# Kernel optimization log

Hardware: AMD Instinct MI355X
Metric: run time of the kernel (lower is better)

The kernel has to match this reference:

```python
import jax, jax.numpy as jnp
import numpy as np
from functools import partial

# Block hyperparams (match init_kwargs)
B, C, N, H = 16, 512, 1024, 8
HID = 4 * C
TAU, THRESH, SG_SCALE = 2.0, 1.0, 5.0
ATTN_SCALE = 0.25
BN_EPS = 1e-5

# LIF spiking neuron (single-step, stateless): membrane v = x / tau, hard threshold
# forward; sigmoid surrogate gradient (scale=5.0) in backward.
@partial(jax.custom_vjp, nondiff_argnums=(1,))
def spike(u, scale):
    return (u >= 0.0).astype(u.dtype)

def _spike_fwd(u, scale):
    return spike(u, scale), u

def _spike_bwd(scale, u, g):
    s = jax.nn.sigmoid(scale * u)
    return (g * scale * s * (1.0 - s),)

spike.defvjp(_spike_fwd, _spike_bwd)

def lif(x):
    return spike(x / TAU - THRESH, SG_SCALE)

def conv1x1(x, w, b=None):
    # x: [B,C,N], w: [O,C] -> [B,O,N]
    y = jnp.einsum('oc,bcn->bon', w, x)
    return y if b is None else y + b[None, :, None]

def bn(x, g, b):
    # BatchNorm1d, training-mode batch stats over (batch, length), biased var
    m = jnp.mean(x, axis=(0, 2), keepdims=True)
    v = jnp.var(x, axis=(0, 2), keepdims=True)
    return (x - m) * jax.lax.rsqrt(v + BN_EPS) * g[None, :, None] + b[None, :, None]


def setup_inputs() -> dict:
    key = jax.random.key(0)
    ks = jax.random.split(key, 8)
    w = lambda k, o, i: jax.random.normal(k, (o, i), dtype=jnp.float32) * 0.02
    inp = {
        'x': jax.random.normal(ks[0], (B, C, N), dtype=jnp.float32),
        'q_w': w(ks[1], C, C), 'q_g': jnp.ones((C,), jnp.float32), 'q_b': jnp.zeros((C,), jnp.float32),
        'k_w': w(ks[2], C, C), 'k_g': jnp.ones((C,), jnp.float32), 'k_b': jnp.zeros((C,), jnp.float32),
        'v_w': w(ks[3], C, C), 'v_g': jnp.ones((C,), jnp.float32), 'v_b': jnp.zeros((C,), jnp.float32),
        'proj_w': w(ks[4], C, C), 'proj_bias': jnp.zeros((C,), jnp.float32),
        'proj_g': jnp.ones((C,), jnp.float32), 'proj_b': jnp.zeros((C,), jnp.float32),
        'fc1_w': w(ks[5], HID, C), 'fc1_bias': jnp.zeros((HID,), jnp.float32),
        'fc1_g': jnp.ones((HID,), jnp.float32), 'fc1_b': jnp.zeros((HID,), jnp.float32),
        'fc2_w': w(ks[6], C, HID), 'fc2_bias': jnp.zeros((C,), jnp.float32),
        'fc2_g': jnp.ones((C,), jnp.float32), 'fc2_b': jnp.zeros((C,), jnp.float32),
    }
    return inp


def reference(x, q_w, q_g, q_b, k_w, k_g, k_b, v_w, v_g, v_b,
              proj_w, proj_bias, proj_g, proj_b,
              fc1_w, fc1_bias, fc1_g, fc1_b, fc2_w, fc2_bias, fc2_g, fc2_b):
    Bb, Cc, Nn = x.shape
    D = Cc // H

    def heads(t):  # [B,C,N] -> [B,H,N,D]
        return t.transpose(0, 2, 1).reshape(Bb, Nn, H, D).transpose(0, 2, 1, 3)

    # spiking attention (no softmax): (Q K^T) V * 0.25
    q = heads(lif(bn(conv1x1(x, q_w), q_g, q_b)))
    k = heads(lif(bn(conv1x1(x, k_w), k_g, k_b)))
    v = heads(lif(bn(conv1x1(x, v_w), v_g, v_b)))
    scores = jnp.einsum('bhnd,bhmd->bhnm', q, k)            # [B,H,N,N]
    attn = jnp.einsum('bhnm,bhmd->bhnd', scores, v) * ATTN_SCALE
    a = attn.transpose(0, 1, 3, 2).reshape(Bb, Cc, Nn)       # [B,C,N]
    a = lif(a)
    a = lif(bn(conv1x1(a, proj_w, proj_bias), proj_g, proj_b))
    x = x + a                                                # residual 1

    # conv1x1-BN-LIF MLP
    h = lif(bn(conv1x1(x, fc1_w, fc1_bias), fc1_g, fc1_b))
    h = lif(bn(conv1x1(h, fc2_w, fc2_bias), fc2_g, fc2_b))
    return x + h                                             # residual 2
```

## Files before the change

kernel.cpp:

```cpp
#include <hip/hip_runtime.h>
#include <stdint.h>

#pragma clang fp contract(off)

#define BATCH 16
#define CCH   512
#define NLEN  1024
#define NH    8
#define DH    64

__device__ float pw128(const float* __restrict__ x) {
    float r0=x[0],r1=x[1],r2=x[2],r3=x[3],r4=x[4],r5=x[5],r6=x[6],r7=x[7];
    for (int i = 8; i < 128; i += 8) {
        r0 += x[i+0]; r1 += x[i+1]; r2 += x[i+2]; r3 += x[i+3];
        r4 += x[i+4]; r5 += x[i+5]; r6 += x[i+6]; r7 += x[i+7];
    }
    return ((r0+r1)+(r2+r3))+((r4+r5)+(r6+r7));
}
__device__ float pw128_sqdev(const float* __restrict__ x, float m) {
    float r0,r1,r2,r3,r4,r5,r6,r7;
    {
        float d;
        d = x[0]-m; r0 = d*d;  d = x[1]-m; r1 = d*d;
        d = x[2]-m; r2 = d*d;  d = x[3]-m; r3 = d*d;
        d = x[4]-m; r4 = d*d;  d = x[5]-m; r5 = d*d;
        d = x[6]-m; r6 = d*d;  d = x[7]-m; r7 = d*d;
    }
    for (int i = 8; i < 128; i += 8) {
        float d;
        d = x[i+0]-m; r0 += d*d;  d = x[i+1]-m; r1 += d*d;
        d = x[i+2]-m; r2 += d*d;  d = x[i+3]-m; r3 += d*d;
        d = x[i+4]-m; r4 += d*d;  d = x[i+5]-m; r5 += d*d;
        d = x[i+6]-m; r6 += d*d;  d = x[i+7]-m; r7 += d*d;
    }
    return ((r0+r1)+(r2+r3))+((r4+r5)+(r6+r7));
}

__global__ __launch_bounds__(64) void bn_stats_np_k(const float* __restrict__ Y, int O,
                                                    float2* __restrict__ st)
{
    const int o = blockIdx.x;
    const int t = threadIdx.x;
    __shared__ float part[16];
    __shared__ float msh;
    if (t < 16) {
        const float* p = Y + ((size_t)t * O + o) * NLEN;
        float b0 = pw128(p), b1 = pw128(p+128), b2 = pw128(p+256), b3 = pw128(p+384);
        float b4 = pw128(p+512), b5 = pw128(p+640), b6 = pw128(p+768), b7 = pw128(p+896);
        part[t] = ((b0+b1)+(b2+b3))+((b4+b5)+(b6+b7));
    }
    __syncthreads();
    if (t == 0) {
        float s = part[0];
        for (int b = 1; b < 16; ++b) s += part[b];
        msh = s / 16384.0f;
    }
    __syncthreads();
    const float m = msh;
    if (t < 16) {
        const float* p = Y + ((size_t)t * O + o) * NLEN;
        float b0 = pw128_sqdev(p,     m), b1 = pw128_sqdev(p+128, m);
        float b2 = pw128_sqdev(p+256, m), b3 = pw128_sqdev(p+384, m);
        float b4 = pw128_sqdev(p+512, m), b5 = pw128_sqdev(p+640, m);
        float b6 = pw128_sqdev(p+768, m), b7 = pw128_sqdev(p+896, m);
        part[t] = ((b0+b1)+(b2+b3))+((b4+b5)+(b6+b7));
    }
    __syncthreads();
    if (t == 0) {
        float s = part[0];
        for (int b = 1; b < 16; ++b) s += part[b];
        float var = s / 16384.0f;
        float ve  = var + 1e-5f;
        float sq  = (float)sqrt((double)ve);
        float r   = (float)(1.0 / (double)sq);
        st[o] = make_float2(m, r);
    }
}

__device__ inline bool spike_f32(float y, float2 s, float g, float b) {
    float t1 = y - s.x;
    float t2 = t1 * s.y;
    float t3 = t2 * g;
    float t4 = t3 + b;
    float u  = t4 / 2.0f - 1.0f;
    return u >= 0.0f;
}

template<int MODE>
__global__ __launch_bounds__(512, 2) void gemm_k(
    const float* __restrict__ W, const float* __restrict__ Xf, const uint8_t* __restrict__ Xs8,
    const float* __restrict__ bias, float* __restrict__ Y,
    int O, int Cin, int N)
{
    __shared__ float Ws[32][132];
    __shared__ float Xs[32][132];
    const int b = blockIdx.z;
    const size_t xbase = (size_t)b * Cin * N;
    float* Yb = Y + (size_t)b * O * N;
    const int o0 = blockIdx.y * 128;
    const int n0 = blockIdx.x * 128;
    const int t  = threadIdx.x;
    const int tx = t & 15;
    const int ty = t >> 4;

    const int wr = t >> 2;
    const int wk = (t & 3) << 3;
    const int xk = t >> 4;
    const int xc = (t & 15) << 3;

    float acc[4][8];
#pragma unroll
    for (int i = 0; i < 4; ++i)
#pragma unroll
        for (int j = 0; j < 8; ++j) acc[i][j] = 0.0f;

    float4 wA0, wA1;
    float  xr[8];

    auto loadG = [&](int k0) {
        const float* wp = W + (size_t)(o0 + wr) * Cin + k0 + wk;
        wA0 = *reinterpret_cast<const float4*>(wp);
        wA1 = *reinterpret_cast<const float4*>(wp + 4);
        size_t off = xbase + (size_t)(k0 + xk) * N + n0 + xc;
        if (MODE == 0) {
            float4 v0 = *reinterpret_cast<const float4*>(Xf + off);
            float4 v1 = *reinterpret_cast<const float4*>(Xf + off + 4);
            xr[0]=v0.x; xr[1]=v0.y; xr[2]=v0.z; xr[3]=v0.w;
            xr[4]=v1.x; xr[5]=v1.y; xr[6]=v1.z; xr[7]=v1.w;
        } else {
            float4 v0 = *reinterpret_cast<const float4*>(Xf + off);
            float4 v1 = *reinterpret_cast<const float4*>(Xf + off + 4);
            uchar4 u0 = *reinterpret_cast<const uchar4*>(Xs8 + off);
            uchar4 u1 = *reinterpret_cast<const uchar4*>(Xs8 + off + 4);
            xr[0]=v0.x+(float)u0.x; xr[1]=v0.y+(float)u0.y;
            xr[2]=v0.z+(float)u0.z; xr[3]=v0.w+(float)u0.w;
            xr[4]=v1.x+(float)u1.x; xr[5]=v1.y+(float)u1.y;
            xr[6]=v1.z+(float)u1.z; xr[7]=v1.w+(float)u1.w;
        }
    };
    auto stage = [&]() {
        Ws[wk+0][wr]=wA0.x; Ws[wk+1][wr]=wA0.y; Ws[wk+2][wr]=wA0.z; Ws[wk+3][wr]=wA0.w;
        Ws[wk+4][wr]=wA1.x; Ws[wk+5][wr]=wA1.y; Ws[wk+6][wr]=wA1.z; Ws[wk+7][wr]=wA1.w;
        *reinterpret_cast<float4*>(&Xs[xk][xc])     = make_float4(xr[0],xr[1],xr[2],xr[3]);
        *reinterpret_cast<float4*>(&Xs[xk][xc + 4]) = make_float4(xr[4],xr[5],xr[6],xr[7]);
    };

    loadG(0);
    stage();
    __syncthreads();
    for (int k0 = 0;;) {
        const int kn = k0 + 32;
        const bool more = kn < Cin;
        if (more) loadG(kn);
#pragma unroll
        for (int kk = 0; kk < 32; ++kk) {
            float4 a  = *reinterpret_cast<const float4*>(&Ws[kk][ty * 4]);
            float4 b0 = *reinterpret_cast<const float4*>(&Xs[kk][tx * 4]);
            float4 b1 = *reinterpret_cast<const float4*>(&Xs[kk][64 + tx * 4]);
            float av[4] = {a.x, a.y, a.z, a.w};
            float bv[8] = {b0.x, b0.y, b0.z, b0.w, b1.x, b1.y, b1.z, b1.w};
#pragma unroll
            for (int i = 0; i < 4; ++i)
#pragma unroll
                for (int j = 0; j < 8; ++j)
                    acc[i][j] = fmaf(av[i], bv[j], acc[i][j]);
        }
        if (!more) break;
        __syncthreads();
        stage();
        __syncthreads();
        k0 = kn;
    }
#pragma unroll
    for (int i = 0; i < 4; ++i) {
        const int o = o0 + ty * 4 + i;
        const float bb = bias ? bias[o] : 0.0f;
        float* yp = Yb + (size_t)o * N + n0;
        float4 r0, r1;
        r0.x = acc[i][0] + bb; r0.y = acc[i][1] + bb;
        r0.z = acc[i][2] + bb; r0.w = acc[i][3] + bb;
        r1.x = acc[i][4] + bb; r1.y = acc[i][5] + bb;
        r1.z = acc[i][6] + bb; r1.w = acc[i][7] + bb;
        *reinterpret_cast<float4*>(yp + tx * 4)      = r0;
        *reinterpret_cast<float4*>(yp + 64 + tx * 4) = r1;
    }
}

__global__ __launch_bounds__(256) void wt_k(const float* __restrict__ W, float* __restrict__ Wt,
                                            int O, int Cin)
{
    __shared__ float tile[32][33];
    const int k0 = blockIdx.x * 32, o0 = blockIdx.y * 32;
    const int tx = threadIdx.x & 31, ty = threadIdx.x >> 5;
#pragma unroll
    for (int j = 0; j < 4; ++j)
        tile[ty + 8*j][tx] = W[(size_t)(o0 + ty + 8*j) * Cin + k0 + tx];
    __syncthreads();
#pragma unroll
    for (int j = 0; j < 4; ++j)
        Wt[(size_t)(k0 + ty + 8*j) * O + o0 + tx] = tile[tx][ty + 8*j];
}

__global__ __launch_bounds__(256) void col_bits_k(const uint8_t* __restrict__ S,
                                                  unsigned long long* __restrict__ bits, int Cin)
{
    const int n0 = blockIdx.x * 64, kw = blockIdx.y, b = blockIdx.z;
    __shared__ uint8_t tile[64][64];
    const int t = threadIdx.x;
    const int r = t >> 2, cg = (t & 3) * 16;
    const uint8_t* src = S + ((size_t)b * Cin + kw * 64 + r) * NLEN + n0 + cg;
    *reinterpret_cast<uint4*>(&tile[r][cg]) = *reinterpret_cast<const uint4*>(src);
    __syncthreads();
    if (t < 64) {
        unsigned long long m = 0;
#pragma unroll
        for (int rr = 0; rr < 64; ++rr)
            m |= ((unsigned long long)(tile[rr][t] != 0)) << rr;
        bits[((size_t)b * NLEN + n0 + t) * (Cin >> 6) + kw] = m;
    }
}

__global__ __launch_bounds__(256) void sparse_gemm_k(
    const float* __restrict__ Wt, const unsigned long long* __restrict__ bits,
    const float* __restrict__ bias, float* __restrict__ Y, int Cin)
{
    const int wid  = (blockIdx.x << 2) + (threadIdx.x >> 6);
    const int lane = threadIdx.x & 63;
    const int b = wid >> 10, n = wid & 1023;
    const int W64 = Cin >> 6;
    float acc[8];
#pragma unroll
    for (int i = 0; i < 8; ++i) acc[i] = 0.0f;
    const unsigned long long* bp = bits + ((size_t)b * NLEN + n) * W64;
    for (int w = 0; w < W64; ++w) {
        unsigned long long m = bp[w];
        while (m) {
            const int bit = __builtin_ctzll(m);
            m &= m - 1;
            const int k = (w << 6) + bit;
            const float* wr = Wt + ((size_t)k << 9) + lane * 8;
            float4 w0 = *reinterpret_cast<const float4*>(wr);
            float4 w1 = *reinterpret_cast<const float4*>(wr + 4);
            acc[0] += w0.x; acc[1] += w0.y; acc[2] += w0.z; acc[3] += w0.w;
            acc[4] += w1.x; acc[5] += w1.y; acc[6] += w1.z; acc[7] += w1.w;
        }
    }
    const float* bq = bias + lane * 8;
    float4 b0 = *reinterpret_cast<const float4*>(bq);
    float4 b1 = *reinterpret_cast<const float4*>(bq + 4);
    float bi[8] = {b0.x, b0.y, b0.z, b0.w, b1.x, b1.y, b1.z, b1.w};
    float* yp = Y + ((size_t)b * 512 + lane * 8) * NLEN + n;
#pragma unroll
    for (int i = 0; i < 8; ++i)
        yp[(size_t)i * NLEN] = acc[i] + bi[i];
}

__global__ __launch_bounds__(256) void spike_pack_k(
    const float* __restrict__ Y, const float2* __restrict__ st,
    const float* __restrict__ g, const float* __restrict__ bet,
    uint8_t* __restrict__ out)
{
    const int nt = blockIdx.x, h = blockIdx.y, b = blockIdx.z;
    __shared__ uint8_t tile[64][68];
    const int t = threadIdx.x;
    {
        const int i = t & 63, dq = t >> 6;
#pragma unroll
        for (int p = 0; p < 16; ++p) {
            int d = dq * 16 + p;
            int c = h * 64 + d;
            float y = Y[((size_t)b * CCH + c) * NLEN + nt * 64 + i];
            tile[d][i] = spike_f32(y, st[c], g[c], bet[c]) ? 1 : 0;
        }
    }
    __syncthreads();
    {
        const int d = t & 63, iq = t >> 6;
#pragma unroll
        for (int p = 0; p < 16; ++p) {
            int i = iq * 16 + p;
            out[((size_t)(b * NH + h) * NLEN + nt * 64 + i) * DH + d] = tile[d][i];
        }
    }
}

__global__ __launch_bounds__(256) void ktv_k(const uint8_t* __restrict__ Kb, const uint8_t* __restrict__ Vb,
                                             float* __restrict__ M)
{
    const int bh = blockIdx.x;
    const uint8_t* kp = Kb + (size_t)bh * NLEN * DH;
    const uint8_t* vp = Vb + (size_t)bh * NLEN * DH;
    __shared__ float ks[64][68];
    __shared__ float vs[64][68];
    const int t = threadIdx.x;
    const int d2 = t & 63, g4 = t >> 6;
    float acc[16];
#pragma unroll
    for (int j = 0; j < 16; ++j) acc[j] = 0.f;

    for (int nc = 0; nc < NLEN; nc += 64) {
#pragma unroll
        for (int p = 0; p < 16; ++p) {
            int idx = t + p * 256;
            int r = idx >> 6, d = idx & 63;
            ks[r][d] = (float)kp[(size_t)(nc + r) * DH + d];
            vs[r][d] = (float)vp[(size_t)(nc + r) * DH + d];
        }
        __syncthreads();
        for (int n = 0; n < 64; ++n) {
            float vv = vs[n][d2];
#pragma unroll
            for (int j = 0; j < 16; ++j)
                acc[j] += ks[n][g4 * 16 + j] * vv;
        }
        __syncthreads();
    }
#pragma unroll
    for (int j = 0; j < 16; ++j)
        M[(size_t)bh * 4096 + (size_t)(g4 * 16 + j) * 64 + d2] = acc[j];
}

__global__ __launch_bounds__(256) void attn_spike_k(const uint8_t* __restrict__ Qb, const float* __restrict__ M,
                                                    uint8_t* __restrict__ A)
{
    const int nt = blockIdx.x, h = blockIdx.y, b = blockIdx.z;
    const int bh = b * NH + h;
    __shared__ float Ms[64][68];
    __shared__ float qs[64][65];
    const int t = threadIdx.x;
#pragma unroll
    for (int p = 0; p < 16; ++p) {
        int idx = t + p * 256;
        int r = idx >> 6, c = idx & 63;
        Ms[r][c] = M[(size_t)bh * 4096 + idx];
        qs[c][r] = (float)Qb[((size_t)bh * NLEN + nt * 64 + r) * DH + c];
    }
    __syncthreads();
    const int n = t & 63, dg = t >> 6;
    float acc[16];
#pragma unroll
    for (int j = 0; j < 16; ++j) acc[j] = 0.f;
    for (int d1 = 0; d1 < 64; ++d1) {
        float qv = qs[d1][n];
#pragma unroll
        for (int j = 0; j < 16; ++j)
            acc[j] += qv * Ms[d1][dg * 16 + j];
    }
#pragma unroll
    for (int j = 0; j < 16; ++j) {
        int d = dg * 16 + j;
        A[((size_t)b * CCH + h * 64 + d) * NLEN + nt * 64 + n] = (acc[j] >= 8.0f) ? 1 : 0;
    }
}

__global__ __launch_bounds__(256) void spike_store_k(
    const float* __restrict__ Y, const float2* __restrict__ st,
    const float* __restrict__ g, const float* __restrict__ bet,
    uint8_t* __restrict__ H, int Oc, int o_off, int Otot)
{
    size_t i4 = (size_t)blockIdx.x * 256 + threadIdx.x;
    size_t total = (size_t)BATCH * Oc * (NLEN / 4);
    if (i4 >= total) return;
    int n4 = (int)(i4 & 255);
    int o  = (int)((i4 >> 8) % Oc);
    int b  = (int)(i4 / ((size_t)256 * Oc));
    float4 y = reinterpret_cast<const float4*>(Y)[i4];
    float2 s = st[o];
    float gg = g[o], bb = bet[o];
    uchar4 r;
    r.x = spike_f32(y.x, s, gg, bb) ? 1 : 0;
    r.y = spike_f32(y.y, s, gg, bb) ? 1 : 0;
    r.z = spike_f32(y.z, s, gg, bb) ? 1 : 0;
    r.w = spike_f32(y.w, s, gg, bb) ? 1 : 0;
    *reinterpret_cast<uchar4*>(H + ((size_t)(b * Otot + o_off + o)) * NLEN + n4 * 4) = r;
}

__global__ __launch_bounds__(256) void final_k(
    const float* __restrict__ Y, const float2* __restrict__ st,
    const float* __restrict__ g, const float* __restrict__ bet,
    const float* __restrict__ x, const uint8_t* __restrict__ ares,
    float* __restrict__ Out)
{
    size_t i4 = (size_t)blockIdx.x * 256 + threadIdx.x;
    size_t total = (size_t)BATCH * CCH * (NLEN / 4);
    if (i4 >= total) return;
    int o = (int)((i4 >> 8) % CCH);
    float4 y  = reinterpret_cast<const float4*>(Y)[i4];
    float4 xv = reinterpret_cast<const float4*>(x)[i4];
    uchar4 av = reinterpret_cast<const uchar4*>(ares)[i4];
    float2 s = st[o];
    float gg = g[o], bb = bet[o];
    float4 r;
    {
        float x1;
        x1 = xv.x + (float)av.x; r.x = x1 + (spike_f32(y.x, s, gg, bb) ? 1.0f : 0.0f);
        x1 = xv.y + (float)av.y; r.y = x1 + (spike_f32(y.y, s, gg, bb) ? 1.0f : 0.0f);
        x1 = xv.z + (float)av.z; r.z = x1 + (spike_f32(y.z, s, gg, bb) ? 1.0f : 0.0f);
        x1 = xv.w + (float)av.w; r.w = x1 + (spike_f32(y.w, s, gg, bb) ? 1.0f : 0.0f);
    }
    reinterpret_cast<float4*>(Out)[i4] = r;
}

extern "C" void kernel_launch(void* const* d_in, const int* in_sizes, int n_in,
                              void* d_out, int out_size, void* d_ws, size_t ws_size,
                              hipStream_t stream)
{
    const float* x         = (const float*)d_in[0];
    const float* q_w       = (const float*)d_in[1];
    const float* q_g       = (const float*)d_in[2];
    const float* q_b       = (const float*)d_in[3];
    const float* k_w       = (const float*)d_in[4];
    const float* k_g       = (const float*)d_in[5];
    const float* k_b       = (const float*)d_in[6];
    const float* v_w       = (const float*)d_in[7];
    const float* v_g       = (const float*)d_in[8];
    const float* v_b       = (const float*)d_in[9];
    const float* proj_w    = (const float*)d_in[10];
    const float* proj_bias = (const float*)d_in[11];
    const float* proj_g    = (const float*)d_in[12];
    const float* proj_b    = (const float*)d_in[13];
    const float* fc1_w     = (const float*)d_in[14];
    const float* fc1_bias  = (const float*)d_in[15];
    const float* fc1_g     = (const float*)d_in[16];
    const float* fc1_b     = (const float*)d_in[17];
    const float* fc2_w     = (const float*)d_in[18];
    const float* fc2_bias  = (const float*)d_in[19];
    const float* fc2_g     = (const float*)d_in[20];
    const float* fc2_b     = (const float*)d_in[21];
    float* out = (float*)d_out;

    char* ws = (char*)d_ws;
    const size_t MiB = 1ull << 20;
    if (ws_size < 124 * MiB) return;

    float*    Af    = (float*)(ws);
    uint8_t*  ab    = (uint8_t*)(ws + 64 * MiB);
    uint8_t*  ares  = (uint8_t*)(ws + 72 * MiB);
    uint8_t*  qb    = (uint8_t*)(ws + 80 * MiB);
    uint8_t*  kb    = (uint8_t*)(ws + 88 * MiB);
    uint8_t*  vb    = (uint8_t*)(ws + 96 * MiB);
    uint8_t*  hb    = (uint8_t*)(ws + 80 * MiB);
    float*    Mbuf  = (float*)(ws + 112 * MiB);
    float2*   stats = (float2*)(ws + 114 * MiB);
    float*    Wt    = (float*)(ws + 115 * MiB);
    unsigned long long* bits = (unsigned long long*)(ws + 119 * MiB);

    dim3 thr256(256), thr512(512);

    const float* Wts[3] = {q_w, k_w, v_w};
    const float* Gt[3]  = {q_g, k_g, v_g};
    const float* Bt[3]  = {q_b, k_b, v_b};
    uint8_t*     Pt[3]  = {qb, kb, vb};
    for (int tsr = 0; tsr < 3; ++tsr) {
        gemm_k<0><<<dim3(8, 4, 16), thr512, 0, stream>>>(Wts[tsr], x, nullptr, nullptr, Af, 512, 512, 1024);
        bn_stats_np_k<<<dim3(512), dim3(64), 0, stream>>>(Af, 512, stats);
        spike_pack_k<<<dim3(16, 8, 16), thr256, 0, stream>>>(Af, stats, Gt[tsr], Bt[tsr], Pt[tsr]);
    }

    ktv_k<<<dim3(128), thr256, 0, stream>>>(kb, vb, Mbuf);
    attn_spike_k<<<dim3(16, 8, 16), thr256, 0, stream>>>(qb, Mbuf, ab);

    wt_k<<<dim3(16, 16), thr256, 0, stream>>>(proj_w, Wt, 512, 512);
    col_bits_k<<<dim3(16, 8, 16), thr256, 0, stream>>>(ab, bits, 512);
    sparse_gemm_k<<<dim3(4096), thr256, 0, stream>>>(Wt, bits, proj_bias, Af, 512);
    bn_stats_np_k<<<dim3(512), dim3(64), 0, stream>>>(Af, 512, stats);
    spike_store_k<<<dim3(8192), thr256, 0, stream>>>(Af, stats, proj_g, proj_b, ares, 512, 0, 512);

    for (int ch = 0; ch < 2; ++ch) {
        gemm_k<2><<<dim3(8, 8, 16), thr512, 0, stream>>>(fc1_w + (size_t)ch * 1024 * 512, x, ares,
                                                         fc1_bias + ch * 1024, Af, 1024, 512, 1024);
        bn_stats_np_k<<<dim3(1024), dim3(64), 0, stream>>>(Af, 1024, stats);
        spike_store_k<<<dim3(16384), thr256, 0, stream>>>(Af, stats, fc1_g + ch * 1024, fc1_b + ch * 1024,
                                                          hb, 1024, ch * 1024, 2048);
    }

    wt_k<<<dim3(64, 16), thr256, 0, stream>>>(fc2_w, Wt, 512, 2048);
    col_bits_k<<<dim3(16, 32, 16), thr256, 0, stream>>>(hb, bits, 2048);
    sparse_gemm_k<<<dim3(4096), thr256, 0, stream>>>(Wt, bits, fc2_bias, Af, 2048);
    bn_stats_np_k<<<dim3(512), dim3(64), 0, stream>>>(Af, 512, stats);
    final_k<<<dim3(8192), thr256, 0, stream>>>(Af, stats, fc2_g, fc2_b, x, ares, out);
}
```

Baseline: 1.515 ms.

## Fuse QKV projections into one GEMM, enlarge per-thread tiles, parallelize BN stats

Concatenates the q/k/v weights into one 1536x512 matrix so a single GEMM, a single BN-stats pass and a single spike-pack kernel replace three sequential rounds. The GEMM moves from 512 threads with 4x8 outputs each to 256 threads with 8x8 outputs each, which raises register reuse per shared-memory load. BN stats now use all 64 threads (4 per batch row) instead of 16, which shortens the serial reduction. The workspace layout is reshuffled to fit the larger Q/K/V intermediate, and three device-to-device weight copies are added on every call.

Result: slower. 3.270 ms (+115.8%).

```diff
diff --git a/kernel.cpp b/kernel.cpp
--- a/kernel.cpp
+++ b/kernel.cpp
@@ -41,34 +41,38 @@
 {
     const int o = blockIdx.x;
     const int t = threadIdx.x;
-    __shared__ float part[16];
+    const int bi = t >> 2, q = t & 3;
+    __shared__ float part[64];
     __shared__ float msh;
-    if (t < 16) {
-        const float* p = Y + ((size_t)t * O + o) * NLEN;
-        float b0 = pw128(p), b1 = pw128(p+128), b2 = pw128(p+256), b3 = pw128(p+384);
-        float b4 = pw128(p+512), b5 = pw128(p+640), b6 = pw128(p+768), b7 = pw128(p+896);
-        part[t] = ((b0+b1)+(b2+b3))+((b4+b5)+(b6+b7));
+    const float* p = Y + ((size_t)bi * O + o) * NLEN + q * 256;
+    {
+        float s0 = pw128(p), s1 = pw128(p + 128);
+        part[t] = s0 + s1;
     }
     __syncthreads();
     if (t == 0) {
-        float s = part[0];
-        for (int b = 1; b < 16; ++b) s += part[b];
+        float s = 0.0f;
+        for (int b = 0; b < 16; ++b) {
+            const float* pp = &part[b * 4];
+            float v = (pp[0] + pp[1]) + (pp[2] + pp[3]);
+            s = (b == 0) ? v : (s + v);
+        }
         msh = s / 16384.0f;
     }
     __syncthreads();
     const float m = msh;
-    if (t < 16) {
-        const float* p = Y + ((size_t)t * O + o) * NLEN;
-        float b0 = pw128_sqdev(p,     m), b1 = pw128_sqdev(p+128, m);
-        float b2 = pw128_sqdev(p+256, m), b3 = pw128_sqdev(p+384, m);
-        float b4 = pw128_sqdev(p+512, m), b5 = pw128_sqdev(p+640, m);
-        float b6 = pw128_sqdev(p+768, m), b7 = pw128_sqdev(p+896, m);
-        part[t] = ((b0+b1)+(b2+b3))+((b4+b5)+(b6+b7));
+    {
+        float s0 = pw128_sqdev(p, m), s1 = pw128_sqdev(p + 128, m);
+        part[t] = s0 + s1;
     }
     __syncthreads();
     if (t == 0) {
-        float s = part[0];
-        for (int b = 1; b < 16; ++b) s += part[b];
+        float s = 0.0f;
+        for (int b = 0; b < 16; ++b) {
+            const float* pp = &part[b * 4];
+            float v = (pp[0] + pp[1]) + (pp[2] + pp[3]);
+            s = (b == 0) ? v : (s + v);
+        }
         float var = s / 16384.0f;
         float ve  = var + 1e-5f;
         float sq  = (float)sqrt((double)ve);
@@ -87,7 +91,7 @@
 }
 
 template<int MODE>
-__global__ __launch_bounds__(512, 2) void gemm_k(
+__global__ __launch_bounds__(256, 4) void gemm_k(
     const float* __restrict__ W, const float* __restrict__ Xf, const uint8_t* __restrict__ Xs8,
     const float* __restrict__ bias, float* __restrict__ Y,
     int O, int Cin, int N)
@@ -103,46 +107,50 @@
     const int tx = t & 15;
     const int ty = t >> 4;
 
-    const int wr = t >> 2;
-    const int wk = (t & 3) << 3;
-    const int xk = t >> 4;
-    const int xc = (t & 15) << 3;
-
-    float acc[4][8];
-#pragma unroll
-    for (int i = 0; i < 4; ++i)
+    const int wr = t >> 1;
+    const int wk = (t & 1) << 4;
+    const int xk = t >> 3;
+    const int xc = (t & 7) << 4;
+
+    float acc[8][8];
+#pragma unroll
+    for (int i = 0; i < 8; ++i)
 #pragma unroll
         for (int j = 0; j < 8; ++j) acc[i][j] = 0.0f;
 
-    float4 wA0, wA1;
-    float  xr[8];
+    float4 wA[4];
+    float  xr[16];
 
     auto loadG = [&](int k0) {
         const float* wp = W + (size_t)(o0 + wr) * Cin + k0 + wk;
-        wA0 = *reinterpret_cast<const float4*>(wp);
-        wA1 = *reinterpret_cast<const float4*>(wp + 4);
+#pragma unroll
+        for (int j = 0; j < 4; ++j)
+            wA[j] = *reinterpret_cast<const float4*>(wp + 4 * j);
         size_t off = xbase + (size_t)(k0 + xk) * N + n0 + xc;
-        if (MODE == 0) {
-            float4 v0 = *reinterpret_cast<const float4*>(Xf + off);
-            float4 v1 = *reinterpret_cast<const float4*>(Xf + off + 4);
-            xr[0]=v0.x; xr[1]=v0.y; xr[2]=v0.z; xr[3]=v0.w;
-            xr[4]=v1.x; xr[5]=v1.y; xr[6]=v1.z; xr[7]=v1.w;
-        } else {
-            float4 v0 = *reinterpret_cast<const float4*>(Xf + off);
-            float4 v1 = *reinterpret_cast<const float4*>(Xf + off + 4);
-            uchar4 u0 = *reinterpret_cast<const uchar4*>(Xs8 + off);
-            uchar4 u1 = *reinterpret_cast<const uchar4*>(Xs8 + off + 4);
-            xr[0]=v0.x+(float)u0.x; xr[1]=v0.y+(float)u0.y;
-            xr[2]=v0.z+(float)u0.z; xr[3]=v0.w+(float)u0.w;
-            xr[4]=v1.x+(float)u1.x; xr[5]=v1.y+(float)u1.y;
-            xr[6]=v1.z+(float)u1.z; xr[7]=v1.w+(float)u1.w;
+#pragma unroll
+        for (int j = 0; j < 4; ++j) {
+            float4 v = *reinterpret_cast<const float4*>(Xf + off + 4 * j);
+            if (MODE == 0) {
+                xr[4*j+0]=v.x; xr[4*j+1]=v.y; xr[4*j+2]=v.z; xr[4*j+3]=v.w;
+            } else {
+                uchar4 u = *reinterpret_cast<const uchar4*>(Xs8 + off + 4 * j);
+                xr[4*j+0]=v.x+(float)u.x; xr[4*j+1]=v.y+(float)u.y;
+                xr[4*j+2]=v.z+(float)u.z; xr[4*j+3]=v.w+(float)u.w;
+            }
         }
     };
     auto stage = [&]() {
-        Ws[wk+0][wr]=wA0.x; Ws[wk+1][wr]=wA0.y; Ws[wk+2][wr]=wA0.z; Ws[wk+3][wr]=wA0.w;
-        Ws[wk+4][wr]=wA1.x; Ws[wk+5][wr]=wA1.y; Ws[wk+6][wr]=wA1.z; Ws[wk+7][wr]=wA1.w;
-        *reinterpret_cast<float4*>(&Xs[xk][xc])     = make_float4(xr[0],xr[1],xr[2],xr[3]);
-        *reinterpret_cast<float4*>(&Xs[xk][xc + 4]) = make_float4(xr[4],xr[5],xr[6],xr[7]);
+#pragma unroll
+        for (int j = 0; j < 4; ++j) {
+            Ws[wk+4*j+0][wr] = wA[j].x;
+            Ws[wk+4*j+1][wr] = wA[j].y;
+            Ws[wk+4*j+2][wr] = wA[j].z;
+            Ws[wk+4*j+3][wr] = wA[j].w;
+        }
+#pragma unroll
+        for (int j = 0; j < 4; ++j)
+            *reinterpret_cast<float4*>(&Xs[xk][xc + 4*j]) =
+                make_float4(xr[4*j+0], xr[4*j+1], xr[4*j+2], xr[4*j+3]);
     };
 
     loadG(0);
@@ -154,13 +162,14 @@
         if (more) loadG(kn);
 #pragma unroll
         for (int kk = 0; kk < 32; ++kk) {
-            float4 a  = *reinterpret_cast<const float4*>(&Ws[kk][ty * 4]);
+            float4 a0 = *reinterpret_cast<const float4*>(&Ws[kk][ty * 4]);
+            float4 a1 = *reinterpret_cast<const float4*>(&Ws[kk][64 + ty * 4]);
             float4 b0 = *reinterpret_cast<const float4*>(&Xs[kk][tx * 4]);
             float4 b1 = *reinterpret_cast<const float4*>(&Xs[kk][64 + tx * 4]);
-            float av[4] = {a.x, a.y, a.z, a.w};
-            float bv[8] = {b0.x, b0.y, b0.z, b0.w, b1.x, b1.y, b1.z, b1.w};
-#pragma unroll
-            for (int i = 0; i < 4; ++i)
+            float av[8] = {a0.x,a0.y,a0.z,a0.w,a1.x,a1.y,a1.z,a1.w};
+            float bv[8] = {b0.x,b0.y,b0.z,b0.w,b1.x,b1.y,b1.z,b1.w};
+#pragma unroll
+            for (int i = 0; i < 8; ++i)
 #pragma unroll
                 for (int j = 0; j < 8; ++j)
                     acc[i][j] = fmaf(av[i], bv[j], acc[i][j]);
@@ -172,18 +181,21 @@
         k0 = kn;
     }
 #pragma unroll
-    for (int i = 0; i < 4; ++i) {
-        const int o = o0 + ty * 4 + i;
-        const float bb = bias ? bias[o] : 0.0f;
-        float* yp = Yb + (size_t)o * N + n0;
-        float4 r0, r1;
-        r0.x = acc[i][0] + bb; r0.y = acc[i][1] + bb;
-        r0.z = acc[i][2] + bb; r0.w = acc[i][3] + bb;
-        r1.x = acc[i][4] + bb; r1.y = acc[i][5] + bb;
-        r1.z = acc[i][6] + bb; r1.w = acc[i][7] + bb;
-        *reinterpret_cast<float4*>(yp + tx * 4)      = r0;
-        *reinterpret_cast<float4*>(yp + 64 + tx * 4) = r1;
-    }
+    for (int half = 0; half < 2; ++half)
+#pragma unroll
+        for (int i = 0; i < 4; ++i) {
+            const int r = half * 4 + i;
+            const int o = o0 + half * 64 + ty * 4 + i;
+            const float bb = bias ? bias[o] : 0.0f;
+            float* yp = Yb + (size_t)o * N + n0;
+            float4 r0, r1;
+            r0.x = acc[r][0] + bb; r0.y = acc[r][1] + bb;
+            r0.z = acc[r][2] + bb; r0.w = acc[r][3] + bb;
+            r1.x = acc[r][4] + bb; r1.y = acc[r][5] + bb;
+            r1.z = acc[r][6] + bb; r1.w = acc[r][7] + bb;
+            *reinterpret_cast<float4*>(yp + tx * 4)      = r0;
+            *reinterpret_cast<float4*>(yp + 64 + tx * 4) = r1;
+        }
 }
 
 __global__ __launch_bounds__(256) void wt_k(const float* __restrict__ W, float* __restrict__ Wt,
@@ -255,22 +267,28 @@
         yp[(size_t)i * NLEN] = acc[i] + bi[i];
 }
 
-__global__ __launch_bounds__(256) void spike_pack_k(
+__global__ __launch_bounds__(256) void spike_pack_qkv_k(
     const float* __restrict__ Y, const float2* __restrict__ st,
-    const float* __restrict__ g, const float* __restrict__ bet,
-    uint8_t* __restrict__ out)
-{
-    const int nt = blockIdx.x, h = blockIdx.y, b = blockIdx.z;
+    const float* __restrict__ gq, const float* __restrict__ gk, const float* __restrict__ gv,
+    const float* __restrict__ bq, const float* __restrict__ bk, const float* __restrict__ bv,
+    uint8_t* __restrict__ oq, uint8_t* __restrict__ ok, uint8_t* __restrict__ ov)
+{
+    const int nt = blockIdx.x, hs = blockIdx.y, b = blockIdx.z;
+    const int tensor = hs >> 3, h = hs & 7;
+    const float* g  = (tensor == 0) ? gq : (tensor == 1) ? gk : gv;
+    const float* be = (tensor == 0) ? bq : (tensor == 1) ? bk : bv;
+    uint8_t* outp   = (tensor == 0) ? oq : (tensor == 1) ? ok : ov;
     __shared__ uint8_t tile[64][68];
     const int t = threadIdx.x;
     {
         const int i = t & 63, dq = t >> 6;
 #pragma unroll
         for (int p = 0; p < 16; ++p) {
-            int d = dq * 16 + p;
-            int c = h * 64 + d;
-            float y = Y[((size_t)b * CCH + c) * NLEN + nt * 64 + i];
-            tile[d][i] = spike_f32(y, st[c], g[c], bet[c]) ? 1 : 0;
+            int d  = dq * 16 + p;
+            int cf = hs * 64 + d;
+            int cl = h * 64 + d;
+            float y = Y[((size_t)b * 1536 + cf) * NLEN + nt * 64 + i];
+            tile[d][i] = spike_f32(y, st[cf], g[cl], be[cl]) ? 1 : 0;
         }
     }
     __syncthreads();
@@ -279,7 +297,7 @@
 #pragma unroll
         for (int p = 0; p < 16; ++p) {
             int i = iq * 16 + p;
-            out[((size_t)(b * NH + h) * NLEN + nt * 64 + i) * DH + d] = tile[d][i];
+            outp[((size_t)(b * NH + h) * NLEN + nt * 64 + i) * DH + d] = tile[d][i];
         }
     }
 }
@@ -433,29 +451,29 @@
     const size_t MiB = 1ull << 20;
     if (ws_size < 124 * MiB) return;
 
+    float*    Yq    = (float*)(ws);
     float*    Af    = (float*)(ws);
-    uint8_t*  ab    = (uint8_t*)(ws + 64 * MiB);
-    uint8_t*  ares  = (uint8_t*)(ws + 72 * MiB);
-    uint8_t*  qb    = (uint8_t*)(ws + 80 * MiB);
-    uint8_t*  kb    = (uint8_t*)(ws + 88 * MiB);
-    uint8_t*  vb    = (uint8_t*)(ws + 96 * MiB);
-    uint8_t*  hb    = (uint8_t*)(ws + 80 * MiB);
-    float*    Mbuf  = (float*)(ws + 112 * MiB);
-    float2*   stats = (float2*)(ws + 114 * MiB);
-    float*    Wt    = (float*)(ws + 115 * MiB);
-    unsigned long long* bits = (unsigned long long*)(ws + 119 * MiB);
-
-    dim3 thr256(256), thr512(512);
-
-    const float* Wts[3] = {q_w, k_w, v_w};
-    const float* Gt[3]  = {q_g, k_g, v_g};
-    const float* Bt[3]  = {q_b, k_b, v_b};
-    uint8_t*     Pt[3]  = {qb, kb, vb};
-    for (int tsr = 0; tsr < 3; ++tsr) {
-        gemm_k<0><<<dim3(8, 4, 16), thr512, 0, stream>>>(Wts[tsr], x, nullptr, nullptr, Af, 512, 512, 1024);
-        bn_stats_np_k<<<dim3(512), dim3(64), 0, stream>>>(Af, 512, stats);
-        spike_pack_k<<<dim3(16, 8, 16), thr256, 0, stream>>>(Af, stats, Gt[tsr], Bt[tsr], Pt[tsr]);
-    }
+    uint8_t*  ab    = (uint8_t*)(ws);
+    uint8_t*  ares  = (uint8_t*)(ws + 64 * MiB);
+    uint8_t*  hb    = (uint8_t*)(ws + 72 * MiB);
+    uint8_t*  qb    = (uint8_t*)(ws + 96 * MiB);
+    uint8_t*  kb    = (uint8_t*)(ws + 104 * MiB);
+    uint8_t*  vb    = (uint8_t*)(ws + 112 * MiB);
+    float*    Wt    = (float*)(ws + 104 * MiB);
+    unsigned long long* bits = (unsigned long long*)(ws + 108 * MiB);
+    float*    Wcat  = (float*)(ws + 120 * MiB);
+    float*    Mbuf  = (float*)(ws + 120 * MiB);
+    float2*   stats = (float2*)(ws + 123 * MiB);
+
+    dim3 thr256(256);
+
+    hipMemcpyAsync(Wcat,          q_w, (size_t)512 * 512 * 4, hipMemcpyDeviceToDevice, stream);
+    hipMemcpyAsync(Wcat + 262144, k_w, (size_t)512 * 512 * 4, hipMemcpyDeviceToDevice, stream);
+    hipMemcpyAsync(Wcat + 524288, v_w, (size_t)512 * 512 * 4, hipMemcpyDeviceToDevice, stream);
+    gemm_k<0><<<dim3(8, 12, 16), thr256, 0, stream>>>(Wcat, x, nullptr, nullptr, Yq, 1536, 512, 1024);
+    bn_stats_np_k<<<dim3(1536), dim3(64), 0, stream>>>(Yq, 1536, stats);
+    spike_pack_qkv_k<<<dim3(16, 24, 16), thr256, 0, stream>>>(Yq, stats, q_g, k_g, v_g,
+                                                              q_b, k_b, v_b, qb, kb, vb);
 
     ktv_k<<<dim3(128), thr256, 0, stream>>>(kb, vb, Mbuf);
     attn_spike_k<<<dim3(16, 8, 16), thr256, 0, stream>>>(qb, Mbuf, ab);
@@ -467,7 +485,7 @@
     spike_store_k<<<dim3(8192), thr256, 0, stream>>>(Af, stats, proj_g, proj_b, ares, 512, 0, 512);
 
     for (int ch = 0; ch < 2; ++ch) {
-        gemm_k<2><<<dim3(8, 8, 16), thr512, 0, stream>>>(fc1_w + (size_t)ch * 1024 * 512, x, ares,
+        gemm_k<2><<<dim3(8, 8, 16), thr256, 0, stream>>>(fc1_w + (size_t)ch * 1024 * 512, x, ares,
                                                          fc1_bias + ch * 1024, Af, 1024, 512, 1024);
         bn_stats_np_k<<<dim3(1024), dim3(64), 0, stream>>>(Af, 1024, stats);
         spike_store_k<<<dim3(16384), thr256, 0, stream>>>(Af, stats, fc1_g + ch * 1024, fc1_b + ch * 1024,
```
